# Optimization experiments

Hardware: AMD Instinct MI355X
Metric: run time of the kernel (lower is better)

The kernel has to match this reference:

```python
import jax, jax.numpy as jnp
import numpy as np

B, L = 2048, 64
STOCH, DETER, OBS, HID, ACT = 30, 200, 200, 200, 6


def setup_inputs() -> dict:
    key = jax.random.key(0)
    ks = jax.random.split(key, 20)
    p = lambda k, shape: jax.random.normal(k, shape, dtype=jnp.float32) * 0.05
    return {
        'obs_feats': jax.random.normal(ks[0], (B, L, OBS), dtype=jnp.float32),
        'actions': jax.random.normal(ks[1], (B, L, ACT), dtype=jnp.float32),
        'noise': jax.random.normal(ks[2], (B, L, STOCH), dtype=jnp.float32),
        # GRUCell params (torch layout: weight [3*deter, in])
        'W_ih': p(ks[3], (3 * DETER, STOCH + ACT)),
        'b_ih': p(ks[4], (3 * DETER,)),
        'W_hh': p(ks[5], (3 * DETER, DETER)),
        'b_hh': p(ks[6], (3 * DETER,)),
        # prior_net: Linear(deter->hid), ReLU, Linear(hid->2*stoch)
        'pW1': p(ks[7], (HID, DETER)), 'pb1': p(ks[8], (HID,)),
        'pW2': p(ks[9], (2 * STOCH, HID)), 'pb2': p(ks[10], (2 * STOCH,)),
        # post_net: Linear(obs+deter->hid), ReLU, Linear(hid->2*stoch)
        'qW1': p(ks[11], (HID, OBS + DETER)), 'qb1': p(ks[12], (HID,)),
        'qW2': p(ks[13], (2 * STOCH, HID)), 'qb2': p(ks[14], (2 * STOCH,)),
        # to_next_s: Linear(stoch->stoch)
        'sW': p(ks[15], (STOCH, STOCH)), 'sb': p(ks[16], (STOCH,)),
    }


def _std(pre):
    return jnp.clip(jax.nn.softplus(pre) + 1e-5, 1e-4)


def reference(obs_feats, actions, noise,
              W_ih, b_ih, W_hh, b_hh,
              pW1, pb1, pW2, pb2,
              qW1, qb1, qW2, qb2,
              sW, sb):
    def step(carry, xs):
        h, s = carry
        obs, a, eps = xs  # [B,OBS], [B,ACT], [B,STOCH]
        x = jnp.concatenate([s, a], axis=-1)  # [B, STOCH+ACT]
        gi = x @ W_ih.T + b_ih
        gh = h @ W_hh.T + b_hh
        ir, iz, inn = jnp.split(gi, 3, axis=-1)
        hr, hz, hn = jnp.split(gh, 3, axis=-1)
        r = jax.nn.sigmoid(ir + hr)
        z = jax.nn.sigmoid(iz + hz)
        n = jnp.tanh(inn + r * hn)
        h_new = (1.0 - z) * n + z * h  # [B, DETER]
        # prior
        pp = jax.nn.relu(h_new @ pW1.T + pb1) @ pW2.T + pb2
        mu_p, pre_p = jnp.split(pp, 2, axis=-1)
        std_p = _std(pre_p)
        # posterior (concat obs_feat and h)
        qp = jax.nn.relu(jnp.concatenate([obs, h_new], axis=-1) @ qW1.T + qb1) @ qW2.T + qb2
        mu_q, pre_q = jnp.split(qp, 2, axis=-1)
        std_q = _std(pre_q)
        s_new = mu_q + std_q * eps  # reparameterize
        return (h_new, s_new), (mu_p, std_p, mu_q, std_q, s_new, h_new)

    h0 = jnp.zeros((obs_feats.shape[0], DETER), dtype=obs_feats.dtype)
    s0 = jnp.zeros((obs_feats.shape[0], STOCH), dtype=obs_feats.dtype)
    xs = (jnp.swapaxes(obs_feats, 0, 1),  # [L,B,OBS]
          jnp.swapaxes(actions, 0, 1),
          jnp.swapaxes(noise, 0, 1))
    _, ys = jax.lax.scan(step, (h0, s0), xs)
    # each y: [L, B, *] -> [B, L, *]; concat along feature dim -> [B, L, 4*STOCH+STOCH+DETER]
    out = jnp.concatenate([jnp.swapaxes(y, 0, 1) for y in ys], axis=-1)
    return out
```

## Files before the change

### kernel.cpp

```cpp
#include <hip/hip_runtime.h>


typedef unsigned short u16;
typedef unsigned int u32;
typedef __attribute__((ext_vector_type(8))) short short8;
typedef __attribute__((ext_vector_type(4))) float f32x4;

#define LL 64
#define OBS_ 200
#define ACT_ 6
#define STO 30
#define OUTC 350

#define U_WG   0
#define U_PW1  468
#define U_QW1  559
#define U_PW2  741
#define U_QW2  769
#define U_TOT  797
#define QX_OFF (1u << 20)

__device__ __forceinline__ u16 f2b(float f){
  u32 u = __float_as_uint(f);
  u = (u + 0x7fffu + ((u >> 16) & 1u)) >> 16;
  return (u16)u;
}
__device__ __forceinline__ float b2f(u16 h){ return __uint_as_float(((u32)h) << 16); }

__device__ __forceinline__ short8 ldA7(const u16* buf, int r, int colStart){
  return *(const short8*)((const char*)buf + r*512 + ((colStart*2) ^ ((r & 7) << 4)));
}
__device__ __forceinline__ void st27(u16* buf, int r, int c, u16 v){
  *(u16*)((char*)buf + r*512 + ((c*2) ^ ((r & 7) << 4))) = v;
}
__device__ __forceinline__ u16 ld27(const u16* buf, int r, int c){
  return *(const u16*)((const char*)buf + r*512 + ((c*2) ^ ((r & 7) << 4)));
}
__device__ __forceinline__ short8 ldA3(const u16* buf, int r, int colStart){
  return *(const short8*)((const char*)buf + r*448 + ((colStart*2) ^ ((r & 3) << 4)));
}
__device__ __forceinline__ void st23(u16* buf, int r, int c, u16 v){
  *(u16*)((char*)buf + r*448 + ((c*2) ^ ((r & 3) << 4))) = v;
}
__device__ __forceinline__ void st8_3(u16* buf, int r, int c8, short8 v){
  *(short8*)((char*)buf + r*448 + ((c8*16) ^ ((r & 3) << 4))) = v;
}
__device__ __forceinline__ short8 ldB(const char* wsb, int unit, int lane){
  return *(const short8*)(wsb + (((size_t)unit) << 10) + ((size_t)lane << 4));
}
__device__ __forceinline__ short8 lwq(const u16* sw, int lu, int lane){
  return *(const short8*)((const char*)sw + ((size_t)lu << 10) + (lane << 4));
}
__device__ __forceinline__ f32x4 mfma(short8 a, short8 b, f32x4 c){
  return __builtin_amdgcn_mfma_f32_16x16x32_bf16(a, b, c, 0, 0, 0);
}
__device__ __forceinline__ float sigm(float x){ return 1.f / (1.f + __expf(-x)); }
__device__ __forceinline__ float tanhf_(float x){
  x = fminf(fmaxf(x, -15.f), 15.f);
  float e = __expf(-2.f * x);
  return (1.f - e) / (1.f + e);
}
__device__ __forceinline__ float softplus_(float x){
  return (x > 20.f) ? x : log1pf(__expf(x));
}
__device__ __forceinline__ short8 pack8(f32x4 a, f32x4 b){
  short8 v;
  v[0]=(short)f2b(a[0]); v[1]=(short)f2b(a[1]); v[2]=(short)f2b(a[2]); v[3]=(short)f2b(a[3]);
  v[4]=(short)f2b(b[0]); v[5]=(short)f2b(b[1]); v[6]=(short)f2b(b[2]); v[7]=(short)f2b(b[3]);
  return v;
}

__global__ __launch_bounds__(512) void pack_w(
    const float* W_ih, const float* W_hh, const float* pW1f, const float* qW1f,
    const float* pW2f, const float* qW2f, u16* wsu)
{
  int u = blockIdx.x;
  int t = threadIdx.x;
  int lane = t >> 3, j = t & 7;
  int nl = lane & 15, kg = lane >> 4;
  float v = 0.f;
  if (u < U_PW1) {
    int nt = u / 9, ks = u % 9;
    int k = ks*32 + kg*8 + j;
    int c = nt*16 + nl;
    int grow, part, coff;
    if (c < 208)      { grow = c;            part = 0; coff = c; }
    else if (c < 416) { grow = 200 + (c-208); part = 0; coff = c-208; }
    else if (c < 624) { grow = 400 + (c-416); part = 1; coff = c-416; }
    else              { grow = 400 + (c-624); part = 2; coff = c-624; }
    if (coff < 200) {
      if (k < 36)                  { if (part != 2) v = W_ih[grow*36 + k]; }
      else if (k >= 64 && k < 264) { if (part != 1) v = W_hh[grow*200 + (k-64)]; }
    }
  } else if (u < U_QW1) {
    int uu = u - U_PW1; int nt = uu / 7, ks = uu % 7;
    int k = ks*32 + kg*8 + j; int n = nt*16 + nl;
    if (n < 200 && k < 200) v = pW1f[n*200 + k];
  } else if (u < U_PW2) {
    int uu = u - U_QW1; int nt = uu / 14, ks = uu % 14;
    int k = ks*32 + kg*8 + j; int n = nt*16 + nl;
    if (n < 200) {
      if (k < 200) v = qW1f[n*400 + k];
      else if (k >= 224 && k < 424) v = qW1f[n*400 + 200 + (k-224)];
    }
  } else {
    bool isQ = (u >= U_QW2);
    int uu = u - (isQ ? U_QW2 : U_PW2); int nt = uu / 7, ks = uu % 7;
    int k = ks*32 + kg*8 + j; int c = nt*16 + nl;
    int row = (c < 32) ? c : 30 + (c - 32);
    bool ok = (c < 32) ? (c < 30) : ((c - 32) < 30);
    const float* W = isQ ? qW2f : pW2f;
    if (ok && k < 200) v = W[row*200 + k];
  }
  wsu[((size_t)u << 9) + lane*8 + j] = f2b(v);
}

__global__ __launch_bounds__(512) void qx_k(
    const float* __restrict__ obs, const float* __restrict__ qb1,
    const char* __restrict__ wsb, u16* __restrict__ qxp)
{
  const int tid = threadIdx.x, w = tid >> 6, lane = tid & 63;
  const int nl = lane & 15, kg = lane >> 4;
  const int r0 = blockIdx.x * 16;
  __shared__ __align__(16) u16 sob[16*224];
  for (int i = tid; i < 16*224; i += 512) sob[i] = 0;
  __syncthreads();
  if (tid < 400) {
    int m = tid / 25, c8 = tid % 25;
    const float* op = obs + (size_t)(r0+m)*OBS_ + c8*8;
    f32x4 a = *(const f32x4*)op, b = *(const f32x4*)(op + 4);
    st8_3(sob, m, c8, pack8(a, b));
  }
  __syncthreads();
#pragma unroll
  for (int qi = 0; qi < 2; ++qi) {
    int tq = w + qi*8;
    if (tq < 13) {
      f32x4 acc{0,0,0,0};
#pragma unroll
      for (int ks = 0; ks < 7; ++ks)
        acc = mfma(ldA3(sob, nl, ks*32 + kg*8), ldB(wsb, U_QW1 + tq*14 + ks, lane), acc);
      int n = tq*16 + nl;
      if (n < 200) {
        float b = qb1[n];
#pragma unroll
        for (int i = 0; i < 4; ++i)
          qxp[(size_t)(r0 + kg*4 + i)*OBS_ + n] = f2b(acc[i] + b);
      }
    }
  }
}

__global__ __launch_bounds__(512) void prior_k(
    const float* __restrict__ pb1, const float* __restrict__ pb2,
    const char* __restrict__ wsb, float* __restrict__ out)
{
  const int tid = threadIdx.x, w = tid >> 6, lane = tid & 63;
  const int nl = lane & 15, kg = lane >> 4;
  const int r0 = blockIdx.x * 16;
  __shared__ __align__(16) u16 shh[16*224];
  __shared__ __align__(16) u16 spp[16*224];
  for (int i = tid; i < 16*224; i += 512) { shh[i] = 0; spp[i] = 0; }
  __syncthreads();
  if (tid < 400) {
    int m = tid / 25, c8 = tid % 25;
    const float* hp = out + (size_t)(r0+m)*OUTC + 150 + c8*8;
    f32x4 a, b;
#pragma unroll
    for (int i = 0; i < 4; ++i) { a[i] = hp[i]; b[i] = hp[4+i]; }
    st8_3(shh, m, c8, pack8(a, b));
  }
  __syncthreads();
#pragma unroll
  for (int qi = 0; qi < 2; ++qi) {
    int tq = w + qi*8;
    if (tq < 13) {
      f32x4 acc{0,0,0,0};
#pragma unroll
      for (int ks = 0; ks < 7; ++ks)
        acc = mfma(ldA3(shh, nl, ks*32 + kg*8), ldB(wsb, U_PW1 + tq*7 + ks, lane), acc);
      int n = tq*16 + nl;
      if (n < 200) {
        float b = pb1[n];
#pragma unroll
        for (int i = 0; i < 4; ++i) {
          float v = acc[i] + b;
          st23(spp, kg*4 + i, n, f2b(v > 0.f ? v : 0.f));
        }
      }
    }
  }
  __syncthreads();
  if (w < 2) {
    f32x4 a0{0,0,0,0}, a1{0,0,0,0};
#pragma unroll
    for (int ks = 0; ks < 7; ++ks) {
      short8 af = ldA3(spp, nl, ks*32 + kg*8);
      a0 = mfma(af, ldB(wsb, U_PW2 + w*7 + ks,     lane), a0);
      a1 = mfma(af, ldB(wsb, U_PW2 + (w+2)*7 + ks, lane), a1);
    }
    int c3 = w*16 + nl;
    if (c3 < 30) {
      float bmu = pb2[c3], bpre = pb2[30 + c3];
#pragma unroll
      for (int i = 0; i < 4; ++i) {
        size_t ob = (size_t)(r0 + kg*4 + i)*OUTC;
        out[ob + c3] = a0[i] + bmu;
        float sp = softplus_(a1[i] + bpre) + 1e-5f;
        out[ob + 30 + c3] = fmaxf(sp, 1e-4f);
      }
    }
  }
}

__global__ __launch_bounds__(512, 2) void rssm_seq(
    const float* __restrict__ act, const float* __restrict__ noise,
    const float* __restrict__ b_ih, const float* __restrict__ b_hh,
    const float* __restrict__ qb2,
    const u16* __restrict__ qxp, const char* __restrict__ wsb,
    float* __restrict__ out)
{
  const int tid  = threadIdx.x;
  const int w    = tid >> 6;
  const int lane = tid & 63;
  const int nl   = lane & 15;
  const int kg   = lane >> 4;
  const int m0   = blockIdx.x * 16;

  __shared__ __align__(16) u16 swq[119*512];
  __shared__ __align__(16) u16 h0 [16*256];
  __shared__ __align__(16) u16 h1 [16*256];
  __shared__ __align__(16) u16 sqq[16*224];

  for (int i = tid; i < 16*256; i += 512) { h0[i]=0; h1[i]=0; }
  for (int i = tid; i < 16*224; i += 512) sqq[i]=0;
  for (int c = tid; c < 119*64; c += 512) {
    int lu = c >> 6, l16 = c & 63;
    int gu = (lu < 91) ? (U_QW1 + (lu/7)*14 + 7 + (lu%7)) : (U_QW2 + (lu - 91));
    *(short8*)((char*)swq + (size_t)c*16) =
        *(const short8*)(wsb + ((size_t)gu << 10) + (l16 << 4));
  }

  const int  cj  = w*16 + nl;
  const bool j2  = (w >= 3);
  const int  tq2 = w + 5;
  const int  cj2 = tq2*16 + nl;
  const bool cj2v = j2 && (cj2 < 200);
  const float bR1 = b_ih[cj]       + b_hh[cj];
  const float bZ1 = b_ih[200 + cj] + b_hh[200 + cj];
  const float bI1 = b_ih[400 + cj];
  const float bH1 = b_hh[400 + cj];
  float bR2=0,bZ2=0,bI2=0,bH2=0;
  if (cj2v) {
    bR2 = b_ih[cj2] + b_hh[cj2];
    bZ2 = b_ih[200+cj2] + b_hh[200+cj2];
    bI2 = b_ih[400+cj2];
    bH2 = b_hh[400+cj2];
  }
  const bool isP3 = (w < 2);
  const int  c3   = w*16 + nl;
  const bool c3v  = isP3 && (c3 < 30);
  float b3mu=0, b3pre=0;
  if (c3v) { b3mu = qb2[c3]; b3pre = qb2[30 + c3]; }
  const int  t2 = (w - 2)*64 + lane;
  const bool isAct = (w == 2 || w == 3) && (t2 < 96);

  __syncthreads();
  if (tid < 96) {
    int m = tid / 6, j = tid % 6;
    st27(h0, m, 230 + j, f2b(act[(size_t)(m0+m)*LL*ACT_ + j]));
  }
  __syncthreads();

#pragma unroll 1
  for (int l = 0; l < LL; ++l) {
    u16* hO = (l & 1) ? h1 : h0;
    u16* hN = (l & 1) ? h0 : h1;
    const size_t outB = (size_t)l*OUTC;

    float ep[4] = {0,0,0,0};
    if (c3v) {
      const float* np = noise + (size_t)(m0 + kg*4)*LL*STO + (size_t)l*STO + c3;
#pragma unroll
      for (int i = 0; i < 4; ++i) ep[i] = np[(size_t)i*LL*STO];
    }
    float qx1[4], qx2[4] = {0,0,0,0};
#pragma unroll
    for (int i = 0; i < 4; ++i)
      qx1[i] = b2f(qxp[((size_t)(m0 + kg*4 + i)*LL + l)*OBS_ + cj]);
    if (cj2v) {
#pragma unroll
      for (int i = 0; i < 4; ++i)
        qx2[i] = b2f(qxp[((size_t)(m0 + kg*4 + i)*LL + l)*OBS_ + cj2]);
    }
    float av = 0.f;
    if (isAct && (l + 1 < LL))
      av = act[((size_t)(m0 + t2/6)*LL + (l+1))*ACT_ + (t2 % 6)];

    short8 a9[9];
#pragma unroll
    for (int ks = 0; ks < 9; ++ks) {
      const int col = (ks < 2) ? (200 + ks*32 + kg*8) : ((ks-2)*32 + kg*8);
      a9[ks] = ldA7(hO, nl, col);
    }
    if (!j2) {
      f32x4 aR{0,0,0,0}, aZ{0,0,0,0}, aI{0,0,0,0}, aH{0,0,0,0};
#pragma unroll
      for (int ks = 0; ks < 9; ++ks) {
        aR = mfma(a9[ks], ldB(wsb, U_WG + w*9 + ks,      lane), aR);
        aZ = mfma(a9[ks], ldB(wsb, U_WG + (13+w)*9 + ks, lane), aZ);
        if (ks < 2) aI = mfma(a9[ks], ldB(wsb, U_WG + (26+w)*9 + ks, lane), aI);
        else        aH = mfma(a9[ks], ldB(wsb, U_WG + (39+w)*9 + ks, lane), aH);
      }
#pragma unroll
      for (int i = 0; i < 4; ++i) {
        int m = kg*4 + i;
        float r = sigm(aR[i] + bR1);
        float z = sigm(aZ[i] + bZ1);
        float n = tanhf_(aI[i] + bI1 + r*(aH[i] + bH1));
        float hold = b2f(ld27(hO, m, cj));
        float hnew = (1.f - z)*n + z*hold;
        st27(hN, m, cj, f2b(hnew));
        out[(size_t)(m0+m)*LL*OUTC + outB + 150 + cj] = hnew;
      }
    } else {
      f32x4 aR1{0,0,0,0}, aZ1{0,0,0,0}, aI1{0,0,0,0}, aH1{0,0,0,0};
      f32x4 aR2{0,0,0,0}, aZ2{0,0,0,0}, aI2{0,0,0,0}, aH2{0,0,0,0};
#pragma unroll
      for (int ks = 0; ks < 9; ++ks) {
        short8 bRa = ldB(wsb, U_WG + w*9 + ks,        lane);
        short8 bRb = ldB(wsb, U_WG + tq2*9 + ks,      lane);
        short8 bZa = ldB(wsb, U_WG + (13+w)*9 + ks,   lane);
        short8 bZb = ldB(wsb, U_WG + (13+tq2)*9 + ks, lane);
        aR1 = mfma(a9[ks], bRa, aR1); aR2 = mfma(a9[ks], bRb, aR2);
        aZ1 = mfma(a9[ks], bZa, aZ1); aZ2 = mfma(a9[ks], bZb, aZ2);
        if (ks < 2) {
          short8 bIa = ldB(wsb, U_WG + (26+w)*9 + ks,   lane);
          short8 bIb = ldB(wsb, U_WG + (26+tq2)*9 + ks, lane);
          aI1 = mfma(a9[ks], bIa, aI1); aI2 = mfma(a9[ks], bIb, aI2);
        } else {
          short8 bHa = ldB(wsb, U_WG + (39+w)*9 + ks,   lane);
          short8 bHb = ldB(wsb, U_WG + (39+tq2)*9 + ks, lane);
          aH1 = mfma(a9[ks], bHa, aH1); aH2 = mfma(a9[ks], bHb, aH2);
        }
      }
#pragma unroll
      for (int i = 0; i < 4; ++i) {
        int m = kg*4 + i;
        float r = sigm(aR1[i] + bR1);
        float z = sigm(aZ1[i] + bZ1);
        float n = tanhf_(aI1[i] + bI1 + r*(aH1[i] + bH1));
        float hold = b2f(ld27(hO, m, cj));
        float hnew = (1.f - z)*n + z*hold;
        st27(hN, m, cj, f2b(hnew));
        out[(size_t)(m0+m)*LL*OUTC + outB + 150 + cj] = hnew;
      }
      if (cj2 < 200) {
#pragma unroll
        for (int i = 0; i < 4; ++i) {
          int m = kg*4 + i;
          float r = sigm(aR2[i] + bR2);
          float z = sigm(aZ2[i] + bZ2);
          float n = tanhf_(aI2[i] + bI2 + r*(aH2[i] + bH2));
          float hold = b2f(ld27(hO, m, cj2));
          float hnew = (1.f - z)*n + z*hold;
          st27(hN, m, cj2, f2b(hnew));
          out[(size_t)(m0+m)*LL*OUTC + outB + 150 + cj2] = hnew;
        }
      }
    }
    __syncthreads();

    {
      short8 g[7];
#pragma unroll
      for (int ks = 0; ks < 7; ++ks) g[ks] = ldA7(hN, nl, ks*32 + kg*8);
      f32x4 aq1{0,0,0,0}, aq2{0,0,0,0};
#pragma unroll
      for (int ks = 0; ks < 7; ++ks) {
        aq1 = mfma(g[ks], lwq(swq, w*7 + ks, lane), aq1);
        if (j2) aq2 = mfma(g[ks], lwq(swq, tq2*7 + ks, lane), aq2);
      }
#pragma unroll
      for (int i = 0; i < 4; ++i) {
        int m = kg*4 + i;
        float v = aq1[i] + qx1[i];
        st23(sqq, m, cj, f2b(v > 0.f ? v : 0.f));
      }
      if (cj2v) {
#pragma unroll
        for (int i = 0; i < 4; ++i) {
          int m = kg*4 + i;
          float v = aq2[i] + qx2[i];
          st23(sqq, m, cj2, f2b(v > 0.f ? v : 0.f));
        }
      }
    }
    __syncthreads();

    if (isP3) {
      f32x4 a0{0,0,0,0}, a1{0,0,0,0};
#pragma unroll
      for (int ks = 0; ks < 7; ++ks) {
        short8 af = ldA3(sqq, nl, ks*32 + kg*8);
        a0 = mfma(af, lwq(swq, 91 + w*7 + ks,     lane), a0);
        a1 = mfma(af, lwq(swq, 91 + (w+2)*7 + ks, lane), a1);
      }
      if (c3 < 30) {
#pragma unroll
        for (int i = 0; i < 4; ++i) {
          int m = kg*4 + i;
          size_t ob = (size_t)(m0+m)*LL*OUTC + outB;
          float mu = a0[i] + b3mu;
          float sp = softplus_(a1[i] + b3pre) + 1e-5f;
          float sd = fmaxf(sp, 1e-4f);
          float s = mu + sd*ep[i];
          out[ob +  60 + c3] = mu;
          out[ob +  90 + c3] = sd;
          out[ob + 120 + c3] = s;
          st27(hN, m, 200 + c3, f2b(s));
        }
      }
    } else if (isAct && (l + 1 < LL)) {
      st27(hN, t2/6, 230 + (t2 % 6), f2b(av));
    }
    __syncthreads();
  }
}

extern "C" void kernel_launch(void* const* d_in, const int* in_sizes, int n_in,
                              void* d_out, int out_size, void* d_ws, size_t ws_size,
                              hipStream_t stream) {
  const float* obs   = (const float*)d_in[0];
  const float* act   = (const float*)d_in[1];
  const float* noise = (const float*)d_in[2];
  const float* W_ih  = (const float*)d_in[3];
  const float* b_ih  = (const float*)d_in[4];
  const float* W_hh  = (const float*)d_in[5];
  const float* b_hh  = (const float*)d_in[6];
  const float* pW1   = (const float*)d_in[7];
  const float* pb1   = (const float*)d_in[8];
  const float* pW2   = (const float*)d_in[9];
  const float* pb2   = (const float*)d_in[10];
  const float* qW1   = (const float*)d_in[11];
  const float* qb1   = (const float*)d_in[12];
  const float* qW2   = (const float*)d_in[13];
  const float* qb2   = (const float*)d_in[14];
  float* out = (float*)d_out;
  u16* qxp = (u16*)((char*)d_ws + QX_OFF);

  pack_w<<<U_TOT, 512, 0, stream>>>(W_ih, W_hh, pW1, qW1, pW2, qW2, (u16*)d_ws);
  qx_k<<<8192, 512, 0, stream>>>(obs, qb1, (const char*)d_ws, qxp);
  rssm_seq<<<128, 512, 0, stream>>>(act, noise, b_ih, b_hh, qb2,
                                    qxp, (const char*)d_ws, out);
  prior_k<<<8192, 512, 0, stream>>>(pb1, pb2, (const char*)d_ws, out);
}
```

Baseline: 616.9 us.

## Overlap previous-step posterior head with current h-recurrence GEMM in scan loop

Splits the GRU gate GEMM so the h-dependent part (W_hh columns) runs before the stochastic-state input is known. The posterior output head of the previous step runs concurrently in the same phase, and its sample is written into the current input buffer before the barrier. The final step's head is peeled after the loop. The step-level dependency chain is intended to shrink, and barriers are replaced with a lighter custom barrier that waits only on LDS counters. The cost is more complex indexing, with noise and output offsets now lagged by one step, and extra MFMAs for the split input part.

```diff
diff --git a/kernel.cpp b/kernel.cpp
--- a/kernel.cpp
+++ b/kernel.cpp
@@ -19,6 +19,12 @@
 #define U_QW2  769
 #define U_TOT  797
 #define QX_OFF (1u << 20)
+
+#define BAR() do { \
+  asm volatile("s_waitcnt lgkmcnt(0)" ::: "memory"); \
+  __builtin_amdgcn_s_barrier(); \
+  __builtin_amdgcn_sched_barrier(0); \
+} while (0)
 
 __device__ __forceinline__ u16 f2b(float f){
   u32 u = __float_as_uint(f);
@@ -276,11 +282,10 @@
   for (int l = 0; l < LL; ++l) {
     u16* hO = (l & 1) ? h1 : h0;
     u16* hN = (l & 1) ? h0 : h1;
-    const size_t outB = (size_t)l*OUTC;
 
     float ep[4] = {0,0,0,0};
-    if (c3v) {
-      const float* np = noise + (size_t)(m0 + kg*4)*LL*STO + (size_t)l*STO + c3;
+    if (c3v && l > 0) {
+      const float* np = noise + (size_t)(m0 + kg*4)*LL*STO + (size_t)(l-1)*STO + c3;
 #pragma unroll
       for (int i = 0; i < 4; ++i) ep[i] = np[(size_t)i*LL*STO];
     }
@@ -297,79 +302,93 @@
     if (isAct && (l + 1 < LL))
       av = act[((size_t)(m0 + t2/6)*LL + (l+1))*ACT_ + (t2 % 6)];
 
-    short8 a9[9];
-#pragma unroll
-    for (int ks = 0; ks < 9; ++ks) {
-      const int col = (ks < 2) ? (200 + ks*32 + kg*8) : ((ks-2)*32 + kg*8);
-      a9[ks] = ldA7(hO, nl, col);
-    }
-    if (!j2) {
-      f32x4 aR{0,0,0,0}, aZ{0,0,0,0}, aI{0,0,0,0}, aH{0,0,0,0};
-#pragma unroll
-      for (int ks = 0; ks < 9; ++ks) {
-        aR = mfma(a9[ks], ldB(wsb, U_WG + w*9 + ks,      lane), aR);
-        aZ = mfma(a9[ks], ldB(wsb, U_WG + (13+w)*9 + ks, lane), aZ);
-        if (ks < 2) aI = mfma(a9[ks], ldB(wsb, U_WG + (26+w)*9 + ks, lane), aI);
-        else        aH = mfma(a9[ks], ldB(wsb, U_WG + (39+w)*9 + ks, lane), aH);
+    short8 a7[7];
+#pragma unroll
+    for (int j = 0; j < 7; ++j) a7[j] = ldA7(hO, nl, j*32 + kg*8);
+
+    f32x4 hr1{0,0,0,0}, hz1{0,0,0,0}, hn1{0,0,0,0};
+    f32x4 hr2{0,0,0,0}, hz2{0,0,0,0}, hn2{0,0,0,0};
+#pragma unroll
+    for (int j = 0; j < 7; ++j) {
+      hr1 = mfma(a7[j], ldB(wsb, U_WG + w*9 + 2 + j,      lane), hr1);
+      hz1 = mfma(a7[j], ldB(wsb, U_WG + (13+w)*9 + 2 + j, lane), hz1);
+      hn1 = mfma(a7[j], ldB(wsb, U_WG + (39+w)*9 + 2 + j, lane), hn1);
+      if (j2) {
+        hr2 = mfma(a7[j], ldB(wsb, U_WG + tq2*9 + 2 + j,      lane), hr2);
+        hz2 = mfma(a7[j], ldB(wsb, U_WG + (13+tq2)*9 + 2 + j, lane), hz2);
+        hn2 = mfma(a7[j], ldB(wsb, U_WG + (39+tq2)*9 + 2 + j, lane), hn2);
+      }
+    }
+    if (isP3 && l > 0) {
+      f32x4 q0{0,0,0,0}, q1a{0,0,0,0};
+#pragma unroll
+      for (int ks = 0; ks < 7; ++ks) {
+        short8 af = ldA3(sqq, nl, ks*32 + kg*8);
+        q0  = mfma(af, lwq(swq, 91 + w*7 + ks,     lane), q0);
+        q1a = mfma(af, lwq(swq, 91 + (w+2)*7 + ks, lane), q1a);
+      }
+      if (c3 < 30) {
+#pragma unroll
+        for (int i = 0; i < 4; ++i) {
+          int m = kg*4 + i;
+          size_t ob = (size_t)(m0+m)*LL*OUTC + (size_t)(l-1)*OUTC;
+          float mu = q0[i] + b3mu;
+          float sp = softplus_(q1a[i] + b3pre) + 1e-5f;
+          float sd = fmaxf(sp, 1e-4f);
+          float s = mu + sd*ep[i];
+          out[ob +  60 + c3] = mu;
+          out[ob +  90 + c3] = sd;
+          out[ob + 120 + c3] = s;
+          st27(hO, m, 200 + c3, f2b(s));
+        }
+      }
+    }
+    BAR();
+
+    {
+      short8 x0 = ldA7(hO, nl, 200 + kg*8);
+      short8 x1 = ldA7(hO, nl, 232 + kg*8);
+      f32x4 aI1{0,0,0,0}, aI2{0,0,0,0};
+      hr1 = mfma(x0, ldB(wsb, U_WG + w*9 + 0,      lane), hr1);
+      hr1 = mfma(x1, ldB(wsb, U_WG + w*9 + 1,      lane), hr1);
+      hz1 = mfma(x0, ldB(wsb, U_WG + (13+w)*9 + 0, lane), hz1);
+      hz1 = mfma(x1, ldB(wsb, U_WG + (13+w)*9 + 1, lane), hz1);
+      aI1 = mfma(x0, ldB(wsb, U_WG + (26+w)*9 + 0, lane), aI1);
+      aI1 = mfma(x1, ldB(wsb, U_WG + (26+w)*9 + 1, lane), aI1);
+      if (j2) {
+        hr2 = mfma(x0, ldB(wsb, U_WG + tq2*9 + 0,      lane), hr2);
+        hr2 = mfma(x1, ldB(wsb, U_WG + tq2*9 + 1,      lane), hr2);
+        hz2 = mfma(x0, ldB(wsb, U_WG + (13+tq2)*9 + 0, lane), hz2);
+        hz2 = mfma(x1, ldB(wsb, U_WG + (13+tq2)*9 + 1, lane), hz2);
+        aI2 = mfma(x0, ldB(wsb, U_WG + (26+tq2)*9 + 0, lane), aI2);
+        aI2 = mfma(x1, ldB(wsb, U_WG + (26+tq2)*9 + 1, lane), aI2);
       }
 #pragma unroll
       for (int i = 0; i < 4; ++i) {
         int m = kg*4 + i;
-        float r = sigm(aR[i] + bR1);
-        float z = sigm(aZ[i] + bZ1);
-        float n = tanhf_(aI[i] + bI1 + r*(aH[i] + bH1));
+        float r = sigm(hr1[i] + bR1);
+        float z = sigm(hz1[i] + bZ1);
+        float n = tanhf_(aI1[i] + bI1 + r*(hn1[i] + bH1));
         float hold = b2f(ld27(hO, m, cj));
         float hnew = (1.f - z)*n + z*hold;
         st27(hN, m, cj, f2b(hnew));
-        out[(size_t)(m0+m)*LL*OUTC + outB + 150 + cj] = hnew;
-      }
-    } else {
-      f32x4 aR1{0,0,0,0}, aZ1{0,0,0,0}, aI1{0,0,0,0}, aH1{0,0,0,0};
-      f32x4 aR2{0,0,0,0}, aZ2{0,0,0,0}, aI2{0,0,0,0}, aH2{0,0,0,0};
-#pragma unroll
-      for (int ks = 0; ks < 9; ++ks) {
-        short8 bRa = ldB(wsb, U_WG + w*9 + ks,        lane);
-        short8 bRb = ldB(wsb, U_WG + tq2*9 + ks,      lane);
-        short8 bZa = ldB(wsb, U_WG + (13+w)*9 + ks,   lane);
-        short8 bZb = ldB(wsb, U_WG + (13+tq2)*9 + ks, lane);
-        aR1 = mfma(a9[ks], bRa, aR1); aR2 = mfma(a9[ks], bRb, aR2);
-        aZ1 = mfma(a9[ks], bZa, aZ1); aZ2 = mfma(a9[ks], bZb, aZ2);
-        if (ks < 2) {
-          short8 bIa = ldB(wsb, U_WG + (26+w)*9 + ks,   lane);
-          short8 bIb = ldB(wsb, U_WG + (26+tq2)*9 + ks, lane);
-          aI1 = mfma(a9[ks], bIa, aI1); aI2 = mfma(a9[ks], bIb, aI2);
-        } else {
-          short8 bHa = ldB(wsb, U_WG + (39+w)*9 + ks,   lane);
-          short8 bHb = ldB(wsb, U_WG + (39+tq2)*9 + ks, lane);
-          aH1 = mfma(a9[ks], bHa, aH1); aH2 = mfma(a9[ks], bHb, aH2);
-        }
-      }
-#pragma unroll
-      for (int i = 0; i < 4; ++i) {
-        int m = kg*4 + i;
-        float r = sigm(aR1[i] + bR1);
-        float z = sigm(aZ1[i] + bZ1);
-        float n = tanhf_(aI1[i] + bI1 + r*(aH1[i] + bH1));
-        float hold = b2f(ld27(hO, m, cj));
-        float hnew = (1.f - z)*n + z*hold;
-        st27(hN, m, cj, f2b(hnew));
-        out[(size_t)(m0+m)*LL*OUTC + outB + 150 + cj] = hnew;
-      }
-      if (cj2 < 200) {
+        out[(size_t)(m0+m)*LL*OUTC + (size_t)l*OUTC + 150 + cj] = hnew;
+      }
+      if (cj2v) {
 #pragma unroll
         for (int i = 0; i < 4; ++i) {
           int m = kg*4 + i;
-          float r = sigm(aR2[i] + bR2);
-          float z = sigm(aZ2[i] + bZ2);
-          float n = tanhf_(aI2[i] + bI2 + r*(aH2[i] + bH2));
+          float r = sigm(hr2[i] + bR2);
+          float z = sigm(hz2[i] + bZ2);
+          float n = tanhf_(aI2[i] + bI2 + r*(hn2[i] + bH2));
           float hold = b2f(ld27(hO, m, cj2));
           float hnew = (1.f - z)*n + z*hold;
           st27(hN, m, cj2, f2b(hnew));
-          out[(size_t)(m0+m)*LL*OUTC + outB + 150 + cj2] = hnew;
+          out[(size_t)(m0+m)*LL*OUTC + (size_t)l*OUTC + 150 + cj2] = hnew;
         }
       }
     }
-    __syncthreads();
+    BAR();
 
     {
       short8 g[7];
@@ -395,36 +414,39 @@
           st23(sqq, m, cj2, f2b(v > 0.f ? v : 0.f));
         }
       }
-    }
-    __syncthreads();
-
-    if (isP3) {
-      f32x4 a0{0,0,0,0}, a1{0,0,0,0};
-#pragma unroll
-      for (int ks = 0; ks < 7; ++ks) {
-        short8 af = ldA3(sqq, nl, ks*32 + kg*8);
-        a0 = mfma(af, lwq(swq, 91 + w*7 + ks,     lane), a0);
-        a1 = mfma(af, lwq(swq, 91 + (w+2)*7 + ks, lane), a1);
-      }
-      if (c3 < 30) {
-#pragma unroll
-        for (int i = 0; i < 4; ++i) {
-          int m = kg*4 + i;
-          size_t ob = (size_t)(m0+m)*LL*OUTC + outB;
-          float mu = a0[i] + b3mu;
-          float sp = softplus_(a1[i] + b3pre) + 1e-5f;
-          float sd = fmaxf(sp, 1e-4f);
-          float s = mu + sd*ep[i];
-          out[ob +  60 + c3] = mu;
-          out[ob +  90 + c3] = sd;
-          out[ob + 120 + c3] = s;
-          st27(hN, m, 200 + c3, f2b(s));
-        }
-      }
-    } else if (isAct && (l + 1 < LL)) {
-      st27(hN, t2/6, 230 + (t2 % 6), f2b(av));
-    }
-    __syncthreads();
+      if (isAct && (l + 1 < LL))
+        st27(hN, t2/6, 230 + (t2 % 6), f2b(av));
+    }
+    BAR();
+  }
+
+  if (isP3) {
+    float ep[4] = {0,0,0,0};
+    if (c3v) {
+      const float* np = noise + (size_t)(m0 + kg*4)*LL*STO + (size_t)(LL-1)*STO + c3;
+#pragma unroll
+      for (int i = 0; i < 4; ++i) ep[i] = np[(size_t)i*LL*STO];
+    }
+    f32x4 q0{0,0,0,0}, q1a{0,0,0,0};
+#pragma unroll
+    for (int ks = 0; ks < 7; ++ks) {
+      short8 af = ldA3(sqq, nl, ks*32 + kg*8);
+      q0  = mfma(af, lwq(swq, 91 + w*7 + ks,     lane), q0);
+      q1a = mfma(af, lwq(swq, 91 + (w+2)*7 + ks, lane), q1a);
+    }
+    if (c3 < 30) {
+#pragma unroll
+      for (int i = 0; i < 4; ++i) {
+        int m = kg*4 + i;
+        size_t ob = (size_t)(m0+m)*LL*OUTC + (size_t)(LL-1)*OUTC;
+        float mu = q0[i] + b3mu;
+        float sp = softplus_(q1a[i] + b3pre) + 1e-5f;
+        float sd = fmaxf(sp, 1e-4f);
+        out[ob +  60 + c3] = mu;
+        out[ob +  90 + c3] = sd;
+        out[ob + 120 + c3] = mu + sd*ep[i];
+      }
+    }
   }
 }
 
```

Measured after the change: 733.0 us. 18.8% more time.
